# Optimization experiments

Hardware: AMD Instinct MI355X
Metric: run time of the kernel (lower is better)

The kernel has to match this reference:

```python
import jax, jax.numpy as jnp
import numpy as np

BIG = 1000000.0
EPS = 1e-06
COST_CLASS, COST_BBOX, COST_GIOU = 1.0, 5.0, 2.0


def sanitize_boxes(boxes):
    # boxes: [..., 4] cxcywh
    boxes = jnp.nan_to_num(boxes, nan=0.0, posinf=1.0, neginf=0.0)
    cx, cy, w, h = jnp.moveaxis(boxes, -1, 0)
    cx = jnp.clip(cx, 0.0, 1.0)
    cy = jnp.clip(cy, 0.0, 1.0)
    w = jnp.clip(w, EPS, 1.0)
    h = jnp.clip(h, EPS, 1.0)
    return jnp.stack([cx, cy, w, h], axis=-1)


def box_cxcywh_to_xyxy(x):
    cx, cy, w, h = jnp.moveaxis(x, -1, 0)
    return jnp.stack([cx - 0.5 * w, cy - 0.5 * h, cx + 0.5 * w, cy + 0.5 * h], axis=-1)


def pairwise_giou(b1, b2):
    # b1: [B, Q, 4] xyxy, b2: [B, T, 4] xyxy -> [B, Q, T]
    area1 = (b1[..., 2] - b1[..., 0]) * (b1[..., 3] - b1[..., 1])  # [B,Q]
    area2 = (b2[..., 2] - b2[..., 0]) * (b2[..., 3] - b2[..., 1])  # [B,T]
    lt = jnp.maximum(b1[:, :, None, :2], b2[:, None, :, :2])  # [B,Q,T,2]
    rb = jnp.minimum(b1[:, :, None, 2:], b2[:, None, :, 2:])
    wh = jnp.clip(rb - lt, 0.0)
    inter = wh[..., 0] * wh[..., 1]  # [B,Q,T]
    union = area1[:, :, None] + area2[:, None, :] - inter
    iou = inter / union
    # enclosing box
    lt_c = jnp.minimum(b1[:, :, None, :2], b2[:, None, :, :2])
    rb_c = jnp.maximum(b1[:, :, None, 2:], b2[:, None, :, 2:])
    wh_c = jnp.clip(rb_c - lt_c, 0.0)
    area_c = wh_c[..., 0] * wh_c[..., 1]
    return iou - (area_c - union) / area_c


def reference(pred_logits, pred_boxes, tgt_labels, tgt_boxes):
    # Batched cost-matrix construction of HungarianMatcher.forward.
    out_logits = jnp.nan_to_num(pred_logits, nan=0.0, posinf=0.0, neginf=0.0)
    out_prob = jax.nn.softmax(out_logits, axis=-1)  # [B,Q,C]
    out_bbox = sanitize_boxes(pred_boxes)           # [B,Q,4]
    t_bbox = sanitize_boxes(tgt_boxes)              # [B,T,4]

    # cost_class[b,q,t] = -out_prob[b,q,tgt_labels[b,t]]
    B, Q, C = out_prob.shape
    T = tgt_labels.shape[1]
    gather_idx = jnp.broadcast_to(tgt_labels[:, None, :], (B, Q, T))
    cost_class = -jnp.take_along_axis(out_prob, gather_idx, axis=2)  # [B,Q,T]

    # L1 cdist in cxcywh space
    cost_bbox = jnp.sum(jnp.abs(out_bbox[:, :, None, :] - t_bbox[:, None, :, :]), axis=-1)

    cost_giou = -pairwise_giou(box_cxcywh_to_xyxy(out_bbox), box_cxcywh_to_xyxy(t_bbox))

    Cmat = COST_CLASS * cost_class + COST_BBOX * cost_bbox + COST_GIOU * cost_giou
    return jnp.nan_to_num(Cmat, nan=BIG, posinf=BIG, neginf=BIG)


def setup_inputs() -> dict:
    key = jax.random.key(0)
    k1, k2, k3, k4 = jax.random.split(key, 4)
    B, Q, C, T = 64, 900, 256, 200
    return {
        "pred_logits": jax.random.normal(k1, (B, Q, C), dtype=jnp.float32),
        "pred_boxes": jax.random.uniform(k2, (B, Q, 4), dtype=jnp.float32),
        "tgt_labels": jax.random.randint(k3, (B, T), 0, C),
        "tgt_boxes": jax.random.uniform(k4, (B, T, 4), dtype=jnp.float32),
    }
```

## Files before the change

### kernel.cpp

```cpp
#include <hip/hip_runtime.h>
#include <math.h>

constexpr int B = 64, Q = 900, C = 256, T = 200;
constexpr float EPSV = 1e-6f;
constexpr int WPB = 4;
constexpr int QPW = 1;
constexpr int QPB = WPB * QPW;
constexpr int NT4 = T / 4;

__device__ __forceinline__ float clampf(float x, float lo, float hi) {
    return fminf(fmaxf(x, lo), hi);
}

#define DPP_ADD_STEP(x, ctrl, row_mask)                                        \
    (x) += __int_as_float(__builtin_amdgcn_update_dpp(                         \
        0, __float_as_int(x), (ctrl), (row_mask), 0xf, true))

__global__ __launch_bounds__(256, 8)
void matcher_kernel(const float* __restrict__ logits,
                    const float* __restrict__ pboxes,
                    const int*   __restrict__ tlabels,
                    const float* __restrict__ tboxes,
                    float* __restrict__ out)
{
    __shared__ float s_exp[WPB][C];

    const int blocks_per_b = Q / QPB;
    const int b    = blockIdx.x / blocks_per_b;
    const int qblk = blockIdx.x % blocks_per_b;
    const int wave = threadIdx.x >> 6;
    const int lane = threadIdx.x & 63;
    const int q    = qblk * QPB + wave;
    const size_t row = (size_t)b * Q + q;

    const float4 lg = ((const float4*)(logits + row * C))[lane];

    const bool act = lane < NT4;
    const int  t0i = act ? 4 * lane : 0;
    const float4* tb_base = (const float4*)(tboxes + b * (T * 4));
    const float4 tbr0 = tb_base[t0i],     tbr1 = tb_base[t0i + 1];
    const float4 tbr2 = tb_base[t0i + 2], tbr3 = tb_base[t0i + 3];
    const int4 labs = *(const int4*)(tlabels + b * T + t0i);
    const float4 pb  = *(const float4*)(pboxes + row * 4);

    float tx0[4], ty0[4], tx1[4], ty1[4], twd[4], tht[4];
    int   cidx[4];
    {
        const float4 tbr[4] = {tbr0, tbr1, tbr2, tbr3};
        const int lbs[4] = {labs.x, labs.y, labs.z, labs.w};
        #pragma unroll
        for (int s = 0; s < 4; ++s) {
            float cx = clampf(tbr[s].x, 0.0f, 1.0f);
            float cy = clampf(tbr[s].y, 0.0f, 1.0f);
            float w  = clampf(tbr[s].z, EPSV, 1.0f);
            float h  = clampf(tbr[s].w, EPSV, 1.0f);
            twd[s] = w;  tht[s] = h;
            tx0[s] = cx - 0.5f * w;  ty0[s] = cy - 0.5f * h;
            tx1[s] = cx + 0.5f * w;  ty1[s] = cy + 0.5f * h;
            cidx[s] = min(max(lbs[s], 0), C - 1);
        }
    }

    const float pcx = clampf(pb.x, 0.0f, 1.0f), pcy = clampf(pb.y, 0.0f, 1.0f);
    const float pw  = clampf(pb.z, EPSV, 1.0f), ph  = clampf(pb.w, EPSV, 1.0f);
    const float px0 = pcx - 0.5f * pw, py0 = pcy - 0.5f * ph;
    const float px1 = pcx + 0.5f * pw, py1 = pcy + 0.5f * ph;
    const float psx = px0 + px1, psy = py0 + py1;
    const float parea = pw * ph;

    float res[4];
    #pragma unroll
    for (int s = 0; s < 4; ++s) {
        float tsx = tx0[s] + tx1[s];
        float tsy = ty0[s] + ty1[s];
        float s1 = fabsf(psx - tsx) + fabsf(psy - tsy);
        float s2 = fabsf(pw - twd[s]) + fabsf(ph - tht[s]);
        float iwr = fminf(px1, tx1[s]) - fmaxf(px0, tx0[s]);
        float ihr = fminf(py1, ty1[s]) - fmaxf(py0, ty0[s]);
        float inter = fmaxf(iwr, 0.0f) * fmaxf(ihr, 0.0f);
        float uni = fmaf(twd[s], tht[s], parea) - inter;
        float cw = (pw + twd[s]) - iwr;
        float ch = (ph + tht[s]) - ihr;
        float ca = cw * ch;
        float num = fmaf(uni, uni, inter * ca);
        float val = num * __builtin_amdgcn_rcpf(uni * ca);
        float cost = fmaf(2.5f, s1, 2.0f);
        cost = fmaf(5.0f, s2, cost);
        res[s] = fmaf(-2.0f, val, cost);
    }

    const float e0 = __expf(lg.x), e1 = __expf(lg.y);
    const float e2 = __expf(lg.z), e3 = __expf(lg.w);
    ((float4*)&s_exp[wave][4 * lane])[0] = make_float4(e0, e1, e2, e3);
    float ss = (e0 + e1) + (e2 + e3);
    DPP_ADD_STEP(ss, 0x111, 0xf);
    DPP_ADD_STEP(ss, 0x112, 0xf);
    DPP_ADD_STEP(ss, 0x114, 0xf);
    DPP_ADD_STEP(ss, 0x118, 0xf);
    DPP_ADD_STEP(ss, 0x142, 0xa);
    DPP_ADD_STEP(ss, 0x143, 0xc);
    const float inv = __builtin_amdgcn_rcpf(__int_as_float(
        __builtin_amdgcn_readlane(__float_as_int(ss), 63)));

    #pragma unroll
    for (int s = 0; s < 4; ++s) {
        res[s] = fmaf(-s_exp[wave][cidx[s]], inv, res[s]);
    }

    if (act) {
        ((float4*)(out + row * T))[lane] =
            make_float4(res[0], res[1], res[2], res[3]);
    }
}

extern "C" void kernel_launch(void* const* d_in, const int* in_sizes, int n_in,
                              void* d_out, int out_size, void* d_ws, size_t ws_size,
                              hipStream_t stream) {
    const float* logits  = (const float*)d_in[0];
    const float* pboxes  = (const float*)d_in[1];
    const int*   tlabels = (const int*)d_in[2];
    const float* tboxes  = (const float*)d_in[3];
    float* out = (float*)d_out;

    const int blocks_per_b = Q / QPB;
    dim3 grid(B * blocks_per_b);
    dim3 block(64 * WPB);
    matcher_kernel<<<grid, block, 0, stream>>>(logits, pboxes, tlabels, tboxes, out);
}
```

Before: 116.6 us.

## Process six query rows per single-wave block with prefetched logits

Each block is now one wave that loops over six consecutive query rows. Target box decoding and label loads are done once and reused across those rows, and the next row's logits and box are prefetched while the current row is computed. A double-buffered shared exp array lets the row loop proceed without block barriers. The cost is fewer, longer-lived waves and a serial per-wave dependency chain, which may reduce the memory-level parallelism available to hide latency.

```diff
diff --git a/kernel.cpp b/kernel.cpp
--- a/kernel.cpp
+++ b/kernel.cpp
@@ -3,9 +3,7 @@
 
 constexpr int B = 64, Q = 900, C = 256, T = 200;
 constexpr float EPSV = 1e-6f;
-constexpr int WPB = 4;
-constexpr int QPW = 1;
-constexpr int QPB = WPB * QPW;
+constexpr int RPB = 6;
 constexpr int NT4 = T / 4;
 
 __device__ __forceinline__ float clampf(float x, float lo, float hi) {
@@ -16,37 +14,34 @@
     (x) += __int_as_float(__builtin_amdgcn_update_dpp(                         \
         0, __float_as_int(x), (ctrl), (row_mask), 0xf, true))
 
-__global__ __launch_bounds__(256, 8)
+__global__ __launch_bounds__(64, 8)
 void matcher_kernel(const float* __restrict__ logits,
                     const float* __restrict__ pboxes,
                     const int*   __restrict__ tlabels,
                     const float* __restrict__ tboxes,
                     float* __restrict__ out)
 {
-    __shared__ float s_exp[WPB][C];
+    __shared__ float s_exp[2][C];
 
-    const int blocks_per_b = Q / QPB;
+    const int blocks_per_b = Q / RPB;
     const int b    = blockIdx.x / blocks_per_b;
-    const int qblk = blockIdx.x % blocks_per_b;
-    const int wave = threadIdx.x >> 6;
-    const int lane = threadIdx.x & 63;
-    const int q    = qblk * QPB + wave;
-    const size_t row = (size_t)b * Q + q;
+    const int rblk = blockIdx.x % blocks_per_b;
+    const int lane = threadIdx.x;
+    const size_t row0 = (size_t)b * Q + rblk * RPB;
 
-    const float4 lg = ((const float4*)(logits + row * C))[lane];
+    float4 lg_cur = ((const float4*)(logits + row0 * C))[lane];
+    float4 pb_cur = *(const float4*)(pboxes + row0 * 4);
 
     const bool act = lane < NT4;
     const int  t0i = act ? 4 * lane : 0;
     const float4* tb_base = (const float4*)(tboxes + b * (T * 4));
-    const float4 tbr0 = tb_base[t0i],     tbr1 = tb_base[t0i + 1];
-    const float4 tbr2 = tb_base[t0i + 2], tbr3 = tb_base[t0i + 3];
+    const float4 tbr[4] = {tb_base[t0i], tb_base[t0i + 1],
+                           tb_base[t0i + 2], tb_base[t0i + 3]};
     const int4 labs = *(const int4*)(tlabels + b * T + t0i);
-    const float4 pb  = *(const float4*)(pboxes + row * 4);
 
     float tx0[4], ty0[4], tx1[4], ty1[4], twd[4], tht[4];
-    int   cidx[4];
+    int   lidx[4];
     {
-        const float4 tbr[4] = {tbr0, tbr1, tbr2, tbr3};
         const int lbs[4] = {labs.x, labs.y, labs.z, labs.w};
         #pragma unroll
         for (int s = 0; s < 4; ++s) {
@@ -57,59 +52,69 @@
             twd[s] = w;  tht[s] = h;
             tx0[s] = cx - 0.5f * w;  ty0[s] = cy - 0.5f * h;
             tx1[s] = cx + 0.5f * w;  ty1[s] = cy + 0.5f * h;
-            cidx[s] = min(max(lbs[s], 0), C - 1);
+            lidx[s] = min(max(lbs[s], 0), C - 1);
         }
     }
 
-    const float pcx = clampf(pb.x, 0.0f, 1.0f), pcy = clampf(pb.y, 0.0f, 1.0f);
-    const float pw  = clampf(pb.z, EPSV, 1.0f), ph  = clampf(pb.w, EPSV, 1.0f);
-    const float px0 = pcx - 0.5f * pw, py0 = pcy - 0.5f * ph;
-    const float px1 = pcx + 0.5f * pw, py1 = pcy + 0.5f * ph;
-    const float psx = px0 + px1, psy = py0 + py1;
-    const float parea = pw * ph;
+    #pragma unroll
+    for (int r = 0; r < RPB; ++r) {
+        float4 lg_nxt, pb_nxt;
+        if (r + 1 < RPB) {
+            lg_nxt = ((const float4*)(logits + (row0 + r + 1) * C))[lane];
+            pb_nxt = *(const float4*)(pboxes + (row0 + r + 1) * 4);
+        }
 
-    float res[4];
-    #pragma unroll
-    for (int s = 0; s < 4; ++s) {
-        float tsx = tx0[s] + tx1[s];
-        float tsy = ty0[s] + ty1[s];
-        float s1 = fabsf(psx - tsx) + fabsf(psy - tsy);
-        float s2 = fabsf(pw - twd[s]) + fabsf(ph - tht[s]);
-        float iwr = fminf(px1, tx1[s]) - fmaxf(px0, tx0[s]);
-        float ihr = fminf(py1, ty1[s]) - fmaxf(py0, ty0[s]);
-        float inter = fmaxf(iwr, 0.0f) * fmaxf(ihr, 0.0f);
-        float uni = fmaf(twd[s], tht[s], parea) - inter;
-        float cw = (pw + twd[s]) - iwr;
-        float ch = (ph + tht[s]) - ihr;
-        float ca = cw * ch;
-        float num = fmaf(uni, uni, inter * ca);
-        float val = num * __builtin_amdgcn_rcpf(uni * ca);
-        float cost = fmaf(2.5f, s1, 2.0f);
-        cost = fmaf(5.0f, s2, cost);
-        res[s] = fmaf(-2.0f, val, cost);
-    }
+        const float e0 = __expf(lg_cur.x), e1 = __expf(lg_cur.y);
+        const float e2 = __expf(lg_cur.z), e3 = __expf(lg_cur.w);
+        ((float4*)&s_exp[r & 1][4 * lane])[0] = make_float4(e0, e1, e2, e3);
+        float ss = (e0 + e1) + (e2 + e3);
+        DPP_ADD_STEP(ss, 0x111, 0xf);
+        DPP_ADD_STEP(ss, 0x112, 0xf);
+        DPP_ADD_STEP(ss, 0x114, 0xf);
+        DPP_ADD_STEP(ss, 0x118, 0xf);
+        DPP_ADD_STEP(ss, 0x142, 0xa);
+        DPP_ADD_STEP(ss, 0x143, 0xc);
+        const float inv = __builtin_amdgcn_rcpf(__int_as_float(
+            __builtin_amdgcn_readlane(__float_as_int(ss), 63)));
 
-    const float e0 = __expf(lg.x), e1 = __expf(lg.y);
-    const float e2 = __expf(lg.z), e3 = __expf(lg.w);
-    ((float4*)&s_exp[wave][4 * lane])[0] = make_float4(e0, e1, e2, e3);
-    float ss = (e0 + e1) + (e2 + e3);
-    DPP_ADD_STEP(ss, 0x111, 0xf);
-    DPP_ADD_STEP(ss, 0x112, 0xf);
-    DPP_ADD_STEP(ss, 0x114, 0xf);
-    DPP_ADD_STEP(ss, 0x118, 0xf);
-    DPP_ADD_STEP(ss, 0x142, 0xa);
-    DPP_ADD_STEP(ss, 0x143, 0xc);
-    const float inv = __builtin_amdgcn_rcpf(__int_as_float(
-        __builtin_amdgcn_readlane(__float_as_int(ss), 63)));
+        const float pcx = clampf(pb_cur.x, 0.0f, 1.0f);
+        const float pcy = clampf(pb_cur.y, 0.0f, 1.0f);
+        const float pw  = clampf(pb_cur.z, EPSV, 1.0f);
+        const float ph  = clampf(pb_cur.w, EPSV, 1.0f);
+        const float px0 = pcx - 0.5f * pw, py0 = pcy - 0.5f * ph;
+        const float px1 = pcx + 0.5f * pw, py1 = pcy + 0.5f * ph;
+        const float psx = px0 + px1, psy = py0 + py1;
+        const float parea = pw * ph;
 
-    #pragma unroll
-    for (int s = 0; s < 4; ++s) {
-        res[s] = fmaf(-s_exp[wave][cidx[s]], inv, res[s]);
-    }
+        float res[4];
+        #pragma unroll
+        for (int s = 0; s < 4; ++s) {
+            const float g = s_exp[r & 1][lidx[s]];
+            const float tsx = tx0[s] + tx1[s];
+            const float tsy = ty0[s] + ty1[s];
+            float t0 = fmaf(-g, inv, 2.0f);
+            float s1 = fabsf(psx - tsx) + fabsf(psy - tsy);
+            float s2 = fabsf(pw - twd[s]) + fabsf(ph - tht[s]);
+            float iwr = fminf(px1, tx1[s]) - fmaxf(px0, tx0[s]);
+            float ihr = fminf(py1, ty1[s]) - fmaxf(py0, ty0[s]);
+            float inter = fmaxf(iwr, 0.0f) * fmaxf(ihr, 0.0f);
+            float uni = fmaf(twd[s], tht[s], parea) - inter;
+            float cw = (pw + twd[s]) - iwr;
+            float ch = (ph + tht[s]) - ihr;
+            float ca = cw * ch;
+            float num = fmaf(uni, uni, inter * ca);
+            float val = num * __builtin_amdgcn_rcpf(uni * ca);
+            float cost = fmaf(2.5f, s1, t0);
+            cost = fmaf(5.0f, s2, cost);
+            res[s] = fmaf(-2.0f, val, cost);
+        }
 
-    if (act) {
-        ((float4*)(out + row * T))[lane] =
-            make_float4(res[0], res[1], res[2], res[3]);
+        if (act) {
+            ((float4*)(out + (row0 + r) * T))[lane] =
+                make_float4(res[0], res[1], res[2], res[3]);
+        }
+
+        if (r + 1 < RPB) { lg_cur = lg_nxt; pb_cur = pb_nxt; }
     }
 }
 
@@ -122,8 +127,8 @@
     const float* tboxes  = (const float*)d_in[3];
     float* out = (float*)d_out;
 
-    const int blocks_per_b = Q / QPB;
+    const int blocks_per_b = Q / RPB;
     dim3 grid(B * blocks_per_b);
-    dim3 block(64 * WPB);
+    dim3 block(64);
     matcher_kernel<<<grid, block, 0, stream>>>(logits, pboxes, tlabels, tboxes, out);
 }
```

Measured after the change: 119.9 us. +2.8%, slower.
